# Performance work log

Measured on AMD Instinct MI355X. Metric: run time of the kernel, lower is better.

Reference implementation:

```python
import jax, jax.numpy as jnp
import numpy as np

B, S, D, H = 2, 2048, 1024, 16
Dh = D // H

def setup_inputs() -> dict:
    key = jax.random.key(0)
    ks = jax.random.split(key, 11)
    def lin(k, fan_in):
        bound = 1.0 / np.sqrt(fan_in)
        kw, kb = jax.random.split(k)
        W = jax.random.uniform(kw, (D, D), jnp.float32, -bound, bound)
        b = jax.random.uniform(kb, (D,), jnp.float32, -bound, bound)
        return W, b
    Wq, bq = lin(ks[0], D)
    Wk, bk = lin(ks[1], D)
    Wv, bv = lin(ks[2], D)
    Wo, bo = lin(ks[3], D)
    Q = jax.random.normal(ks[4], (B, S, D), jnp.float32)
    K = jax.random.normal(ks[5], (B, S, D), jnp.float32)
    V = jax.random.normal(ks[6], (B, S, D), jnp.float32)
    return {"Q": Q, "K": K, "V": V, "Wq": Wq, "bq": bq, "Wk": Wk, "bk": bk,
            "Wv": Wv, "bv": bv, "Wo": Wo, "bo": bo}

def _split_heads(x):
    # [B,S,D] -> [B,H,S,Dh]
    b, s, _ = x.shape
    return x.reshape(b, s, H, Dh).transpose(0, 2, 1, 3)

def reference(Q, K, V, Wq, bq, Wk, bk, Wv, bv, Wo, bo):
    q = _split_heads(Q @ Wq.T + bq)
    k = _split_heads(K @ Wk.T + bk)
    v = _split_heads(V @ Wv.T + bv)
    scores = jnp.einsum('bhqd,bhkd->bhqk', q, k) / jnp.sqrt(jnp.float32(Dh))
    attn = jax.nn.softmax(scores, axis=-1)
    out = jnp.einsum('bhqk,bhkd->bhqd', attn, v)  # [B,H,S,Dh]
    out = out.transpose(0, 2, 1, 3).reshape(Q.shape[0], Q.shape[1], D)
    return out @ Wo.T + bo
```

## Files before the change

kernel.cpp:

```cpp
#include <hip/hip_runtime.h>

#define SEQ 2048
#define DMODEL 1024
#define NH 16
#define DH 64

typedef __attribute__((ext_vector_type(8))) short bf16x8;
typedef __attribute__((ext_vector_type(4))) short bf16x4;
typedef __attribute__((ext_vector_type(4))) float floatx4;
typedef __attribute__((ext_vector_type(4))) unsigned short u16x4;
typedef unsigned short u16;
typedef unsigned int u32;

typedef const void __attribute__((address_space(1)))* as1cvp;
typedef void __attribute__((address_space(3)))* as3vp;

__device__ __forceinline__ void glds16(const void* g, void* l) {
    __builtin_amdgcn_global_load_lds((as1cvp)g, (as3vp)l, 16, 0, 0);
}

__device__ __forceinline__ u16 f2bf(float f) {
    union { u32 u; float f; } v; v.f = f;
    return (u16)((v.u + 0x8000u) >> 16);
}

__device__ __forceinline__ u32 pk2(float a, float b) {
    union { u32 u; float f; } x, y; x.f = a; y.f = b;
    u32 xr = x.u + 0x8000u, yr = y.u + 0x8000u;
#if __has_builtin(__builtin_amdgcn_perm)
    return __builtin_amdgcn_perm(yr, xr, 0x07060302u);
#else
    return (xr >> 16) | (yr & 0xffff0000u);
#endif
}

__device__ __forceinline__ float ex2(float x) {
#if __has_builtin(__builtin_amdgcn_exp2f)
    return __builtin_amdgcn_exp2f(x);
#else
    float r; asm("v_exp_f32 %0, %1" : "=v"(r) : "v"(x)); return r;
#endif
}

__device__ __forceinline__ floatx4 mfma16(bf16x4 a, bf16x4 b, floatx4 c) {
#if __has_builtin(__builtin_amdgcn_mfma_f32_16x16x16bf16_1k)
    return __builtin_amdgcn_mfma_f32_16x16x16bf16_1k(a, b, c, 0, 0, 0);
#else
    asm volatile("v_mfma_f32_16x16x16_bf16 %0, %1, %2, %0" : "+v"(c) : "v"(a), "v"(b));
    return c;
#endif
}

__device__ __forceinline__ uint4 cvt8(const float* __restrict__ p) {
    float4 a = *(const float4*)p;
    float4 b = *(const float4*)(p + 4);
    uint4 q;
    q.x = pk2(a.x, a.y); q.y = pk2(a.z, a.w);
    q.z = pk2(b.x, b.y); q.w = pk2(b.z, b.w);
    return q;
}

#define QSCALE 0.18033688011112042f

__global__ __launch_bounds__(256) void cvt_all(
    const float* __restrict__ Q, const float* __restrict__ K, const float* __restrict__ V,
    const float* __restrict__ W0, const float* __restrict__ W1,
    const float* __restrict__ W2, const float* __restrict__ W3,
    u16* __restrict__ Qb, u16* __restrict__ Kb, u16* __restrict__ Vb,
    u16* __restrict__ Wb)
{
    const int y = blockIdx.y;
    const float* src; u16* dst;
    if (y == 0)      { src = Q;  dst = Qb; }
    else if (y == 1) { src = K;  dst = Kb; }
    else if (y == 2) { src = V;  dst = Vb; }
    else {
        if (blockIdx.x >= 512) return;
        src = (y == 3) ? W0 : (y == 4) ? W1 : (y == 5) ? W2 : W3;
        dst = Wb + (size_t)(y - 3) * 1048576;
    }
    size_t i = ((size_t)blockIdx.x * 256 + threadIdx.x) * 8;
    *(uint4*)(dst + i) = cvt8(src + i);
}

__global__ __launch_bounds__(256) void cvt_w(
    const float* __restrict__ W0, const float* __restrict__ W1,
    const float* __restrict__ W2, const float* __restrict__ W3,
    u16* __restrict__ out)
{
    const float* src = (blockIdx.y == 0) ? W0 : (blockIdx.y == 1) ? W1
                     : (blockIdx.y == 2) ? W2 : W3;
    size_t i = ((size_t)blockIdx.x * 256 + threadIdx.x) * 8;
    *(uint4*)(out + (size_t)blockIdx.y * 1048576 + i) = cvt8(src + i);
}

__device__ __forceinline__ void qkv_store(
    int z, u16* __restrict__ outp, int rowg, int col, floatx4 a4, float bv, float sc)
{
    union { u32 w[2]; u16 h[4]; u16x4 v4; } pk;
    pk.w[0] = pk2((a4[0] + bv) * sc, (a4[1] + bv) * sc);
    pk.w[1] = pk2((a4[2] + bv) * sc, (a4[3] + bv) * sc);
    int b = rowg >> 11, s = rowg & 2047, h = col >> 6, d = col & 63;
    if (z < 2) {
#pragma unroll
        for (int r = 0; r < 4; r++)
            outp[((size_t)(b * NH + h) * SEQ + s + r) * DH + d] = pk.h[r];
    } else {
        *(u16x4*)(outp + ((size_t)(b * NH + h) * DH + d) * SEQ + s) = pk.v4;
    }
}

__global__ __launch_bounds__(256) void gemm_qkv_bb(
    const u16* __restrict__ Qb, const u16* __restrict__ Kb, const u16* __restrict__ Vb,
    const u16* __restrict__ Wb,
    const float* __restrict__ b0, const float* __restrict__ b1, const float* __restrict__ b2,
    u16* __restrict__ qo, u16* __restrict__ ko, u16* __restrict__ vto)
{
    __shared__ __align__(16) u16 As[3][4096];
    __shared__ __align__(16) u16 Bs[3][4096];
    const int tid = threadIdx.x, l = tid & 63, w = tid >> 6;
    const int lm = l & 15, quad = l >> 4;
    const int wr = (w >> 1) * 64, wc = (w & 1) * 64;
    const int bm = blockIdx.y * 128, bn = blockIdx.x * 128;
    const int z = blockIdx.z;
    const u16* A      = (z == 0) ? Qb : (z == 1) ? Kb : Vb;
    const u16* W      = Wb + (size_t)z * 1048576;
    const float* bias = (z == 0) ? b0 : (z == 1) ? b1 : b2;

    const int srow = tid >> 2, scol = (tid & 3) * 8;

    floatx4 acc[4][4];
#pragma unroll
    for (int i = 0; i < 4; i++)
#pragma unroll
        for (int j = 0; j < 4; j++) acc[i][j] = (floatx4){0.f, 0.f, 0.f, 0.f};

#define QKV_STAGE(I, NB) do { \
        const int kt_ = (I) * 32; \
        glds16(A + (size_t)(bm + srow) * DMODEL + kt_ + scol, As[NB] + w * 512); \
        glds16(A + (size_t)(bm + 64 + srow) * DMODEL + kt_ + scol, As[NB] + 2048 + w * 512); \
        glds16(W + (size_t)(bn + srow) * DMODEL + kt_ + scol, Bs[NB] + w * 512); \
        glds16(W + (size_t)(bn + 64 + srow) * DMODEL + kt_ + scol, Bs[NB] + 2048 + w * 512); \
    } while (0)

    QKV_STAGE(0, 0);
    QKV_STAGE(1, 1);
    asm volatile("s_waitcnt vmcnt(4)" ::: "memory");
    __builtin_amdgcn_s_barrier();

    int cur = 0, nx = 2;
    for (int i = 0; i < 32; i++) {
        bf16x8 af[4], bfr[4];
#pragma unroll
        for (int mi = 0; mi < 4; mi++)
            af[mi] = *(const bf16x8*)(As[cur] + (wr + mi * 16 + lm) * 32 + quad * 8);
#pragma unroll
        for (int ni = 0; ni < 4; ni++)
            bfr[ni] = *(const bf16x8*)(Bs[cur] + (wc + ni * 16 + lm) * 32 + quad * 8);
#pragma unroll
        for (int mi = 0; mi < 4; mi++)
#pragma unroll
            for (int ni = 0; ni < 4; ni++)
                acc[mi][ni] = __builtin_amdgcn_mfma_f32_16x16x32_bf16(
                    af[mi], bfr[ni], acc[mi][ni], 0, 0, 0);

        if (i + 2 < 32) {
            QKV_STAGE(i + 2, nx);
            asm volatile("s_waitcnt vmcnt(4)" ::: "memory");
            __builtin_amdgcn_s_barrier();
        } else if (i + 1 < 32) {
            asm volatile("s_waitcnt vmcnt(0)" ::: "memory");
            __builtin_amdgcn_s_barrier();
        }
        cur = (cur == 2) ? 0 : cur + 1;
        nx  = (nx == 2) ? 0 : nx + 1;
    }
#undef QKV_STAGE

    const float sc = (z == 0) ? QSCALE : 1.0f;
    u16* outp = (z == 0) ? qo : (z == 1) ? ko : vto;
#pragma unroll
    for (int ni = 0; ni < 4; ni++) {
        int col = bn + wc + ni * 16 + lm;
        float bv = bias[col];
#pragma unroll
        for (int mi = 0; mi < 4; mi++)
            qkv_store(z, outp, bm + wr + mi * 16 + quad * 4, col, acc[mi][ni], bv, sc);
    }
}

template<bool WBF>
__global__ __launch_bounds__(256) void gemm_qkv(
    const float* __restrict__ Qf, const float* __restrict__ Kf, const float* __restrict__ Vf,
    const void* __restrict__ W0, const void* __restrict__ W1, const void* __restrict__ W2,
    const float* __restrict__ b0, const float* __restrict__ b1, const float* __restrict__ b2,
    u16* __restrict__ qo, u16* __restrict__ ko, u16* __restrict__ vto)
{
    __shared__ __align__(16) u16 As[128 * 32];
    __shared__ __align__(16) u16 Bs[128 * 32];
    const int tid = threadIdx.x, l = tid & 63, w = tid >> 6;
    const int lm = l & 15, quad = l >> 4;
    const int wr = (w >> 1) * 64, wc = (w & 1) * 64;
    const int bm = blockIdx.y * 128, bn = blockIdx.x * 128;
    const int z = blockIdx.z;
    const float* A    = (z == 0) ? Qf : (z == 1) ? Kf : Vf;
    const void* Wp    = (z == 0) ? W0 : (z == 1) ? W1 : W2;
    const float* bias = (z == 0) ? b0 : (z == 1) ? b1 : b2;

    floatx4 acc[4][4];
#pragma unroll
    for (int i = 0; i < 4; i++)
#pragma unroll
        for (int j = 0; j < 4; j++) acc[i][j] = (floatx4){0.f, 0.f, 0.f, 0.f};

    for (int kt = 0; kt < DMODEL; kt += 32) {
        __syncthreads();
#pragma unroll
        for (int j = 0; j < 2; j++) {
            int ch = j * 256 + tid, row = ch >> 2, c = ch & 3;
            *(uint4*)(As + ch * 8) = cvt8(A + (size_t)(bm + row) * DMODEL + kt + c * 8);
        }
        if (WBF) {
            const u16* Wb = (const u16*)Wp;
            glds16(Wb + (size_t)(bn + (tid >> 2)) * DMODEL + kt + (tid & 3) * 8, Bs + w * 512);
            glds16(Wb + (size_t)(bn + 64 + (tid >> 2)) * DMODEL + kt + (tid & 3) * 8, Bs + 2048 + w * 512);
        } else {
            const float* Wf = (const float*)Wp;
#pragma unroll
            for (int j = 0; j < 2; j++) {
                int ch = j * 256 + tid, row = ch >> 2, c = ch & 3;
                *(uint4*)(Bs + ch * 8) = cvt8(Wf + (size_t)(bn + row) * DMODEL + kt + c * 8);
            }
        }
        __syncthreads();

        bf16x8 af[4], bfr[4];
#pragma unroll
        for (int mi = 0; mi < 4; mi++)
            af[mi] = *(const bf16x8*)(As + (wr + mi * 16 + lm) * 32 + quad * 8);
#pragma unroll
        for (int ni = 0; ni < 4; ni++)
            bfr[ni] = *(const bf16x8*)(Bs + (wc + ni * 16 + lm) * 32 + quad * 8);
#pragma unroll
        for (int mi = 0; mi < 4; mi++)
#pragma unroll
            for (int ni = 0; ni < 4; ni++)
                acc[mi][ni] = __builtin_amdgcn_mfma_f32_16x16x32_bf16(
                    af[mi], bfr[ni], acc[mi][ni], 0, 0, 0);
    }

    const float sc = (z == 0) ? QSCALE : 1.0f;
    u16* outp = (z == 0) ? qo : (z == 1) ? ko : vto;
#pragma unroll
    for (int ni = 0; ni < 4; ni++) {
        int col = bn + wc + ni * 16 + lm;
        float bv = bias[col];
#pragma unroll
        for (int mi = 0; mi < 4; mi++)
            qkv_store(z, outp, bm + wr + mi * 16 + quad * 4, col, acc[mi][ni], bv, sc);
    }
}

__global__ __launch_bounds__(256) void gemm_o_p(
    const u16* __restrict__ A, const u16* __restrict__ W,
    const float* __restrict__ bias, float* __restrict__ out)
{
    __shared__ __align__(16) u16 As[3][4096];
    __shared__ __align__(16) u16 Bs[3][2048];
    const int tid = threadIdx.x, l = tid & 63, w = tid >> 6;
    const int lm = l & 15, quad = l >> 4;
    const int bm = blockIdx.y * 128, bn = blockIdx.x * 64;

    floatx4 acc[2][4];
#pragma unroll
    for (int i = 0; i < 2; i++)
#pragma unroll
        for (int j = 0; j < 4; j++) acc[i][j] = (floatx4){0.f, 0.f, 0.f, 0.f};

#define O_STAGE(I, NB) do { \
        const int kt_ = (I) * 32; \
        glds16(A + (size_t)(bm + (tid >> 2)) * DMODEL + kt_ + (tid & 3) * 8, As[NB] + w * 512); \
        glds16(A + (size_t)(bm + 64 + (tid >> 2)) * DMODEL + kt_ + (tid & 3) * 8, As[NB] + 2048 + w * 512); \
        glds16(W + (size_t)(bn + (tid >> 2)) * DMODEL + kt_ + (tid & 3) * 8, Bs[NB] + w * 512); \
    } while (0)

    O_STAGE(0, 0);
    O_STAGE(1, 1);
    asm volatile("s_waitcnt vmcnt(3)" ::: "memory");
    __builtin_amdgcn_s_barrier();

    int cur = 0, nx = 2;
    for (int i = 0; i < 32; i++) {
        bf16x8 af[2], bfr[4];
#pragma unroll
        for (int mi = 0; mi < 2; mi++)
            af[mi] = *(const bf16x8*)(As[cur] + (w * 32 + mi * 16 + lm) * 32 + quad * 8);
#pragma unroll
        for (int ni = 0; ni < 4; ni++)
            bfr[ni] = *(const bf16x8*)(Bs[cur] + (ni * 16 + lm) * 32 + quad * 8);
#pragma unroll
        for (int mi = 0; mi < 2; mi++)
#pragma unroll
            for (int ni = 0; ni < 4; ni++)
                acc[mi][ni] = __builtin_amdgcn_mfma_f32_16x16x32_bf16(
                    af[mi], bfr[ni], acc[mi][ni], 0, 0, 0);

        if (i + 2 < 32) {
            O_STAGE(i + 2, nx);
            asm volatile("s_waitcnt vmcnt(3)" ::: "memory");
            __builtin_amdgcn_s_barrier();
        } else if (i + 1 < 32) {
            asm volatile("s_waitcnt vmcnt(0)" ::: "memory");
            __builtin_amdgcn_s_barrier();
        }
        cur = (cur == 2) ? 0 : cur + 1;
        nx  = (nx == 2) ? 0 : nx + 1;
    }
#undef O_STAGE

#pragma unroll
    for (int ni = 0; ni < 4; ni++) {
        int col = bn + ni * 16 + lm;
        float bv = bias[col];
#pragma unroll
        for (int mi = 0; mi < 2; mi++) {
#pragma unroll
            for (int r = 0; r < 4; r++) {
                int rowg = bm + w * 32 + mi * 16 + quad * 4 + r;
                out[(size_t)rowg * DMODEL + col] = acc[mi][ni][r] + bv;
            }
        }
    }
}

template<bool WBF>
__global__ __launch_bounds__(256) void gemm_o(
    const u16* __restrict__ A, const void* __restrict__ Wp,
    const float* __restrict__ bias, float* __restrict__ out)
{
    __shared__ __align__(16) u16 As[128 * 32];
    __shared__ __align__(16) u16 Bs[64 * 32];
    const int tid = threadIdx.x, l = tid & 63, w = tid >> 6;
    const int lm = l & 15, quad = l >> 4;
    const int bm = blockIdx.y * 128, bn = blockIdx.x * 64;

    floatx4 acc[2][4];
#pragma unroll
    for (int i = 0; i < 2; i++)
#pragma unroll
        for (int j = 0; j < 4; j++) acc[i][j] = (floatx4){0.f, 0.f, 0.f, 0.f};

    for (int kt = 0; kt < DMODEL; kt += 32) {
        __syncthreads();
        glds16(A + (size_t)(bm + (tid >> 2)) * DMODEL + kt + (tid & 3) * 8, As + w * 512);
        glds16(A + (size_t)(bm + 64 + (tid >> 2)) * DMODEL + kt + (tid & 3) * 8, As + 2048 + w * 512);
        if (WBF) {
            glds16((const u16*)Wp + (size_t)(bn + (tid >> 2)) * DMODEL + kt + (tid & 3) * 8, Bs + w * 512);
        } else {
            *(uint4*)(Bs + tid * 8) =
                cvt8((const float*)Wp + (size_t)(bn + (tid >> 2)) * DMODEL + kt + (tid & 3) * 8);
        }
        __syncthreads();

        bf16x8 af[2], bfr[4];
#pragma unroll
        for (int mi = 0; mi < 2; mi++)
            af[mi] = *(const bf16x8*)(As + (w * 32 + mi * 16 + lm) * 32 + quad * 8);
#pragma unroll
        for (int ni = 0; ni < 4; ni++)
            bfr[ni] = *(const bf16x8*)(Bs + (ni * 16 + lm) * 32 + quad * 8);
#pragma unroll
        for (int mi = 0; mi < 2; mi++)
#pragma unroll
            for (int ni = 0; ni < 4; ni++)
                acc[mi][ni] = __builtin_amdgcn_mfma_f32_16x16x32_bf16(
                    af[mi], bfr[ni], acc[mi][ni], 0, 0, 0);
    }

#pragma unroll
    for (int ni = 0; ni < 4; ni++) {
        int col = bn + ni * 16 + lm;
        float bv = bias[col];
#pragma unroll
        for (int mi = 0; mi < 2; mi++) {
#pragma unroll
            for (int r = 0; r < 4; r++) {
                int rowg = bm + w * 32 + mi * 16 + quad * 4 + r;
                out[(size_t)rowg * DMODEL + col] = acc[mi][ni][r] + bv;
            }
        }
    }
}

#define SP 72
#define TS (64 * SP)
#define BUFSZ (4 * TS)
__global__ __launch_bounds__(512, 4) void attn_kernel(
    const u16* __restrict__ q, const u16* __restrict__ k,
    const u16* __restrict__ vt, u16* __restrict__ out)
{
    __shared__ __align__(16) u16 smem[2 * BUFSZ];
    const int tid = threadIdx.x, l = tid & 63, w = tid >> 6;
    const int lm = l & 15, quad = l >> 4;
    const int qt = blockIdx.x, bh = blockIdx.y;
    const int b = bh >> 4, h = bh & 15;
    const int rg = w & 3, half = w >> 2;

    bf16x8 qf[2][2];
#pragma unroll
    for (int nt = 0; nt < 2; nt++) {
        int row = qt * 128 + rg * 32 + nt * 16 + lm;
        const u16* qp = q + ((size_t)bh * SEQ + row) * DH;
        qf[nt][0] = *(const bf16x8*)(qp + quad * 8);
        qf[nt][1] = *(const bf16x8*)(qp + 32 + quad * 8);
    }

    floatx4 O[4][2];
#pragma unroll
    for (int dt = 0; dt < 4; dt++)
#pragma unroll
        for (int nt = 0; nt < 2; nt++) O[dt][nt] = (floatx4){0.f, 0.f, 0.f, 0.f};
    floatx4 Ol[2] = {(floatx4){0.f,0.f,0.f,0.f}, (floatx4){0.f,0.f,0.f,0.f}};

    const bf16x4 onesb = {(short)0x3F80, (short)0x3F80, (short)0x3F80, (short)0x3F80};

    const int srow = tid >> 3, scol = (tid & 7) * 8;
    const int pb0 = ((scol >> 2) & 3) * 16 + (scol >> 4) * 4;
    const u16* kbase = k + (size_t)bh * SEQ * DH;
    const u16* vbase = vt + (size_t)bh * DH * SEQ;

    uint4 krA, krB, vrA, vrB;
#define LOADT(T) do { \
        const u16* kg = kbase + (size_t)(T) * 64 * DH; \
        const u16* vg = vbase + (size_t)(T) * 64; \
        krA = *(const uint4*)(kg + (size_t)srow * DH + scol); \
        krB = *(const uint4*)(kg + (size_t)(1024 + srow) * DH + scol); \
        vrA = *(const uint4*)(vg + (size_t)srow * SEQ + scol); \
        vrB = *(const uint4*)(vg + (size_t)srow * SEQ + 1024 + scol); \
    } while (0)
#define WRBUF(BUF) do { \
        u16* K0 = smem + (BUF) * BUFSZ; \
        u16* K1 = K0 + TS; \
        u16* V0 = K0 + 2 * TS; \
        u16* V1 = K0 + 3 * TS; \
        *(uint4*)(K0 + srow * SP + scol) = krA; \
        *(uint4*)(K1 + srow * SP + scol) = krB; \
        *(uint2*)(V0 + srow * SP + pb0)      = make_uint2(vrA.x, vrA.y); \
        *(uint2*)(V0 + srow * SP + pb0 + 16) = make_uint2(vrA.z, vrA.w); \
        *(uint2*)(V1 + srow * SP + pb0)      = make_uint2(vrB.x, vrB.y); \
        *(uint2*)(V1 + srow * SP + pb0 + 16) = make_uint2(vrB.z, vrB.w); \
    } while (0)

    LOADT(0);
    WRBUF(0);
    LOADT(1);
    asm volatile("s_waitcnt lgkmcnt(0)" ::: "memory");
    __builtin_amdgcn_s_barrier();

    for (int t = 0; t < 16; t++) {
        const int cur = t & 1;
        const u16* Kh = smem + cur * BUFSZ + half * TS;
        const u16* Vh = smem + cur * BUFSZ + (2 + half) * TS;

        floatx4 Sc[4][2];
        __builtin_amdgcn_s_setprio(1);
#pragma unroll
        for (int mt = 0; mt < 4; mt++) {
            bf16x8 ka0 = *(const bf16x8*)(Kh + (mt * 16 + lm) * SP + quad * 8);
            bf16x8 ka1 = *(const bf16x8*)(Kh + (mt * 16 + lm) * SP + 32 + quad * 8);
#pragma unroll
            for (int nt = 0; nt < 2; nt++) {
                floatx4 c = (floatx4){0.f, 0.f, 0.f, 0.f};
                c = __builtin_amdgcn_mfma_f32_16x16x32_bf16(ka0, qf[nt][0], c, 0, 0, 0);
                c = __builtin_amdgcn_mfma_f32_16x16x32_bf16(ka1, qf[nt][1], c, 0, 0, 0);
                Sc[mt][nt] = c;
            }
        }
        __builtin_amdgcn_s_setprio(0);

        bf16x4 pb[4][2];
#pragma unroll
        for (int nt = 0; nt < 2; nt++) {
#pragma unroll
            for (int mt = 0; mt < 4; mt++) {
#pragma unroll
                for (int r = 0; r < 4; r++) Sc[mt][nt][r] = ex2(Sc[mt][nt][r]);
                union { u32 w2[2]; bf16x4 v; } pku;
                pku.w2[0] = pk2(Sc[mt][nt][0], Sc[mt][nt][1]);
                pku.w2[1] = pk2(Sc[mt][nt][2], Sc[mt][nt][3]);
                pb[mt][nt] = pku.v;
            }
        }

        __builtin_amdgcn_s_setprio(1);
#pragma unroll
        for (int nt = 0; nt < 2; nt++) {
            Ol[nt] = mfma16(onesb, pb[0][nt], Ol[nt]);
            Ol[nt] = mfma16(onesb, pb[1][nt], Ol[nt]);
            Ol[nt] = mfma16(onesb, pb[2][nt], Ol[nt]);
            Ol[nt] = mfma16(onesb, pb[3][nt], Ol[nt]);
        }

#pragma unroll
        for (int dt = 0; dt < 4; dt++) {
            const u16* vp = Vh + (dt * 16 + lm) * SP + quad * 16;
            bf16x8 v8a = *(const bf16x8*)vp;
            bf16x8 v8b = *(const bf16x8*)(vp + 8);
            bf16x4 va0 = __builtin_shufflevector(v8a, v8a, 0, 1, 2, 3);
            bf16x4 va1 = __builtin_shufflevector(v8a, v8a, 4, 5, 6, 7);
            bf16x4 va2 = __builtin_shufflevector(v8b, v8b, 0, 1, 2, 3);
            bf16x4 va3 = __builtin_shufflevector(v8b, v8b, 4, 5, 6, 7);
            O[dt][0] = mfma16(va0, pb[0][0], O[dt][0]);
            O[dt][1] = mfma16(va0, pb[0][1], O[dt][1]);
            O[dt][0] = mfma16(va1, pb[1][0], O[dt][0]);
            O[dt][1] = mfma16(va1, pb[1][1], O[dt][1]);
            O[dt][0] = mfma16(va2, pb[2][0], O[dt][0]);
            O[dt][1] = mfma16(va2, pb[2][1], O[dt][1]);
            O[dt][0] = mfma16(va3, pb[3][0], O[dt][0]);
            O[dt][1] = mfma16(va3, pb[3][1], O[dt][1]);
        }
        __builtin_amdgcn_s_setprio(0);

        if (t + 1 < 16) {
            asm volatile("s_waitcnt vmcnt(0)" ::: "memory");
            WRBUF(cur ^ 1);
            if (t + 2 < 16) LOADT(t + 2);
        }
        asm volatile("s_waitcnt lgkmcnt(0)" ::: "memory");
        __builtin_amdgcn_s_barrier();
    }
#undef LOADT
#undef WRBUF

    float* obuf  = (float*)smem;
    float* mlbuf = (float*)smem + 8192;
    if (w >= 4) {
#pragma unroll
        for (int nt = 0; nt < 2; nt++) {
            float* ob = obuf + (((rg * 64 + l) * 2 + nt) << 4);
#pragma unroll
            for (int dt = 0; dt < 4; dt++)
                *(floatx4*)(ob + dt * 4) = O[dt][nt];
            mlbuf[(rg * 64 + l) * 2 + nt] = Ol[nt][0];
        }
    }
    __syncthreads();
    if (w < 4) {
#pragma unroll
        for (int nt = 0; nt < 2; nt++) {
            float* ob = obuf + (((rg * 64 + l) * 2 + nt) << 4);
            float lB = mlbuf[(rg * 64 + l) * 2 + nt];
            float inv = 1.0f / (Ol[nt][0] + lB);
            int s = qt * 128 + rg * 32 + nt * 16 + lm;
            u16* op = out + ((size_t)b * SEQ + s) * DMODEL + h * DH;
#pragma unroll
            for (int dt = 0; dt < 4; dt++) {
                floatx4 Ob = *(const floatx4*)(ob + dt * 4);
                union { u32 w2[2]; u16x4 v; } pku;
                pku.w2[0] = pk2((O[dt][nt][0] + Ob[0]) * inv,
                                (O[dt][nt][1] + Ob[1]) * inv);
                pku.w2[1] = pk2((O[dt][nt][2] + Ob[2]) * inv,
                                (O[dt][nt][3] + Ob[3]) * inv);
                *(u16x4*)(op + dt * 16 + quad * 4) = pku.v;
            }
        }
    }
}

extern "C" void kernel_launch(void* const* d_in, const int* in_sizes, int n_in,
                              void* d_out, int out_size, void* d_ws, size_t ws_size,
                              hipStream_t stream) {
    (void)in_sizes; (void)n_in; (void)out_size;
    const float* Q  = (const float*)d_in[0];
    const float* K  = (const float*)d_in[1];
    const float* V  = (const float*)d_in[2];
    const float* Wq = (const float*)d_in[3];
    const float* bq = (const float*)d_in[4];
    const float* Wk = (const float*)d_in[5];
    const float* bk = (const float*)d_in[6];
    const float* Wv = (const float*)d_in[7];
    const float* bv = (const float*)d_in[8];
    const float* Wo = (const float*)d_in[9];
    const float* bo = (const float*)d_in[10];

    const size_t NEL = (size_t)2 * NH * SEQ * DH;
    u16* base = (u16*)d_ws;
    dim3 bb(256);
    dim3 ab(512);

    if (ws_size >= 8 * NEL * 2) {
        u16* Qb   = base;
        u16* Kb   = Qb + NEL;
        u16* Vb   = Kb + NEL;
        u16* Wb   = Vb + NEL;
        u16* qws  = Wb + NEL;
        u16* kws  = qws + NEL;
        u16* vtws = kws + NEL;
        u16* aws  = vtws + NEL;
        cvt_all<<<dim3(2048, 7), bb, 0, stream>>>(Q, K, V, Wq, Wk, Wv, Wo, Qb, Kb, Vb, Wb);
        gemm_qkv_bb<<<dim3(8, 32, 3), bb, 0, stream>>>(
            Qb, Kb, Vb, Wb, bq, bk, bv, qws, kws, vtws);
        attn_kernel<<<dim3(SEQ / 128, 2 * NH), ab, 0, stream>>>(qws, kws, vtws, aws);
        gemm_o_p<<<dim3(16, 32), bb, 0, stream>>>(aws, Wb + 3145728, bo, (float*)d_out);
    } else if (ws_size >= 5 * NEL * 2) {
        u16* Wb = base;
        u16* qws = base + NEL; u16* kws = qws + NEL; u16* vtws = kws + NEL; u16* aws = vtws + NEL;
        cvt_w<<<dim3(512, 4), bb, 0, stream>>>(Wq, Wk, Wv, Wo, Wb);
        gemm_qkv<true><<<dim3(8, 32, 3), bb, 0, stream>>>(
            Q, K, V, Wb, Wb + 1048576, Wb + 2097152, bq, bk, bv, qws, kws, vtws);
        attn_kernel<<<dim3(SEQ / 128, 2 * NH), ab, 0, stream>>>(qws, kws, vtws, aws);
        gemm_o_p<<<dim3(16, 32), bb, 0, stream>>>(aws, Wb + 3145728, bo, (float*)d_out);
    } else {
        u16* qws = base; u16* kws = qws + NEL; u16* vtws = kws + NEL; u16* aws = vtws + NEL;
        gemm_qkv<false><<<dim3(8, 32, 3), bb, 0, stream>>>(
            Q, K, V, Wq, Wk, Wv, bq, bk, bv, qws, kws, vtws);
        attn_kernel<<<dim3(SEQ / 128, 2 * NH), ab, 0, stream>>>(qws, kws, vtws, aws);
        gemm_o<false><<<dim3(16, 32), bb, 0, stream>>>(aws, Wo, bo, (float*)d_out);
    }
}
```

Measured before the change: 227.6 us.

## Fuse fp32-to-bf16 activation conversion into pipelined QKV projection GEMM

Removes the separate pass that converted Q/K/V activations to bf16. The QKV GEMM now reads fp32 activations through registers, packs them to bf16 and writes them to a double-buffered LDS tile, while weight tiles keep using a triple-buffered direct global-to-LDS pipeline. This saves one full write and re-read of the bf16 activations. In exchange the A tiles go through registers, so each K step waits on vmcnt(0), and the kernel asks for two blocks per CU through launch bounds.

After: 249.5 us. +9.6%, slower.

```diff
diff --git a/kernel.cpp b/kernel.cpp
--- a/kernel.cpp
+++ b/kernel.cpp
@@ -61,27 +61,6 @@
 }
 
 #define QSCALE 0.18033688011112042f
-
-__global__ __launch_bounds__(256) void cvt_all(
-    const float* __restrict__ Q, const float* __restrict__ K, const float* __restrict__ V,
-    const float* __restrict__ W0, const float* __restrict__ W1,
-    const float* __restrict__ W2, const float* __restrict__ W3,
-    u16* __restrict__ Qb, u16* __restrict__ Kb, u16* __restrict__ Vb,
-    u16* __restrict__ Wb)
-{
-    const int y = blockIdx.y;
-    const float* src; u16* dst;
-    if (y == 0)      { src = Q;  dst = Qb; }
-    else if (y == 1) { src = K;  dst = Kb; }
-    else if (y == 2) { src = V;  dst = Vb; }
-    else {
-        if (blockIdx.x >= 512) return;
-        src = (y == 3) ? W0 : (y == 4) ? W1 : (y == 5) ? W2 : W3;
-        dst = Wb + (size_t)(y - 3) * 1048576;
-    }
-    size_t i = ((size_t)blockIdx.x * 256 + threadIdx.x) * 8;
-    *(uint4*)(dst + i) = cvt8(src + i);
-}
 
 __global__ __launch_bounds__(256) void cvt_w(
     const float* __restrict__ W0, const float* __restrict__ W1,
@@ -110,24 +89,25 @@
     }
 }
 
-__global__ __launch_bounds__(256) void gemm_qkv_bb(
-    const u16* __restrict__ Qb, const u16* __restrict__ Kb, const u16* __restrict__ Vb,
+__global__ __launch_bounds__(256, 2) void gemm_qkv_f32a(
+    const float* __restrict__ Qf, const float* __restrict__ Kf, const float* __restrict__ Vf,
     const u16* __restrict__ Wb,
     const float* __restrict__ b0, const float* __restrict__ b1, const float* __restrict__ b2,
     u16* __restrict__ qo, u16* __restrict__ ko, u16* __restrict__ vto)
 {
-    __shared__ __align__(16) u16 As[3][4096];
+    __shared__ __align__(16) u16 As[2][4096];
     __shared__ __align__(16) u16 Bs[3][4096];
     const int tid = threadIdx.x, l = tid & 63, w = tid >> 6;
     const int lm = l & 15, quad = l >> 4;
     const int wr = (w >> 1) * 64, wc = (w & 1) * 64;
     const int bm = blockIdx.y * 128, bn = blockIdx.x * 128;
     const int z = blockIdx.z;
-    const u16* A      = (z == 0) ? Qb : (z == 1) ? Kb : Vb;
+    const float* A    = (z == 0) ? Qf : (z == 1) ? Kf : Vf;
     const u16* W      = Wb + (size_t)z * 1048576;
     const float* bias = (z == 0) ? b0 : (z == 1) ? b1 : b2;
 
-    const int srow = tid >> 2, scol = (tid & 3) * 8;
+    const int arow = tid >> 1, acol = (tid & 1) * 16;
+    const int wrow = tid >> 2, wcol = (tid & 3) * 8;
 
     floatx4 acc[4][4];
 #pragma unroll
@@ -135,28 +115,42 @@
 #pragma unroll
         for (int j = 0; j < 4; j++) acc[i][j] = (floatx4){0.f, 0.f, 0.f, 0.f};
 
-#define QKV_STAGE(I, NB) do { \
-        const int kt_ = (I) * 32; \
-        glds16(A + (size_t)(bm + srow) * DMODEL + kt_ + scol, As[NB] + w * 512); \
-        glds16(A + (size_t)(bm + 64 + srow) * DMODEL + kt_ + scol, As[NB] + 2048 + w * 512); \
-        glds16(W + (size_t)(bn + srow) * DMODEL + kt_ + scol, Bs[NB] + w * 512); \
-        glds16(W + (size_t)(bn + 64 + srow) * DMODEL + kt_ + scol, Bs[NB] + 2048 + w * 512); \
+    float4 a0, a1, a2, a3;
+#define LOADA(I) do { \
+        const float* ap = A + (size_t)(bm + arow) * DMODEL + (I) * 32 + acol; \
+        a0 = *(const float4*)ap;       a1 = *(const float4*)(ap + 4); \
+        a2 = *(const float4*)(ap + 8); a3 = *(const float4*)(ap + 12); \
     } while (0)
-
-    QKV_STAGE(0, 0);
-    QKV_STAGE(1, 1);
-    asm volatile("s_waitcnt vmcnt(4)" ::: "memory");
+#define STW(I, NB) do { \
+        glds16(W + (size_t)(bn + wrow) * DMODEL + (I) * 32 + wcol, Bs[NB] + w * 512); \
+        glds16(W + (size_t)(bn + 64 + wrow) * DMODEL + (I) * 32 + wcol, Bs[NB] + 2048 + w * 512); \
+    } while (0)
+#define WRA(NB) do { \
+        uint4 c0, c1; \
+        c0.x = pk2(a0.x, a0.y); c0.y = pk2(a0.z, a0.w); \
+        c0.z = pk2(a1.x, a1.y); c0.w = pk2(a1.z, a1.w); \
+        c1.x = pk2(a2.x, a2.y); c1.y = pk2(a2.z, a2.w); \
+        c1.z = pk2(a3.x, a3.y); c1.w = pk2(a3.z, a3.w); \
+        *(uint4*)(As[NB] + arow * 32 + acol)     = c0; \
+        *(uint4*)(As[NB] + arow * 32 + acol + 8) = c1; \
+    } while (0)
+
+    LOADA(0); STW(0, 0);
+    asm volatile("s_waitcnt vmcnt(0)" ::: "memory");
+    WRA(0);
+    LOADA(1); STW(1, 1);
+    asm volatile("s_waitcnt lgkmcnt(0)" ::: "memory");
     __builtin_amdgcn_s_barrier();
 
-    int cur = 0, nx = 2;
+    int curB = 0;
     for (int i = 0; i < 32; i++) {
         bf16x8 af[4], bfr[4];
 #pragma unroll
         for (int mi = 0; mi < 4; mi++)
-            af[mi] = *(const bf16x8*)(As[cur] + (wr + mi * 16 + lm) * 32 + quad * 8);
+            af[mi] = *(const bf16x8*)(As[i & 1] + (wr + mi * 16 + lm) * 32 + quad * 8);
 #pragma unroll
         for (int ni = 0; ni < 4; ni++)
-            bfr[ni] = *(const bf16x8*)(Bs[cur] + (wc + ni * 16 + lm) * 32 + quad * 8);
+            bfr[ni] = *(const bf16x8*)(Bs[curB] + (wc + ni * 16 + lm) * 32 + quad * 8);
 #pragma unroll
         for (int mi = 0; mi < 4; mi++)
 #pragma unroll
@@ -164,18 +158,22 @@
                 acc[mi][ni] = __builtin_amdgcn_mfma_f32_16x16x32_bf16(
                     af[mi], bfr[ni], acc[mi][ni], 0, 0, 0);
 
-        if (i + 2 < 32) {
-            QKV_STAGE(i + 2, nx);
-            asm volatile("s_waitcnt vmcnt(4)" ::: "memory");
-            __builtin_amdgcn_s_barrier();
-        } else if (i + 1 < 32) {
+        if (i + 1 < 32) {
             asm volatile("s_waitcnt vmcnt(0)" ::: "memory");
-            __builtin_amdgcn_s_barrier();
-        }
-        cur = (cur == 2) ? 0 : cur + 1;
-        nx  = (nx == 2) ? 0 : nx + 1;
-    }
-#undef QKV_STAGE
+            WRA((i + 1) & 1);
+            if (i + 2 < 32) {
+                LOADA(i + 2);
+                int nb = curB + 2; nb = (nb >= 3) ? nb - 3 : nb;
+                STW(i + 2, nb);
+            }
+        }
+        asm volatile("s_waitcnt lgkmcnt(0)" ::: "memory");
+        __builtin_amdgcn_s_barrier();
+        curB = (curB == 2) ? 0 : curB + 1;
+    }
+#undef LOADA
+#undef STW
+#undef WRA
 
     const float sc = (z == 0) ? QSCALE : 1.0f;
     u16* outp = (z == 0) ? qo : (z == 1) ? ko : vto;
@@ -221,9 +219,9 @@
             *(uint4*)(As + ch * 8) = cvt8(A + (size_t)(bm + row) * DMODEL + kt + c * 8);
         }
         if (WBF) {
-            const u16* Wb = (const u16*)Wp;
-            glds16(Wb + (size_t)(bn + (tid >> 2)) * DMODEL + kt + (tid & 3) * 8, Bs + w * 512);
-            glds16(Wb + (size_t)(bn + 64 + (tid >> 2)) * DMODEL + kt + (tid & 3) * 8, Bs + 2048 + w * 512);
+            const u16* Wc = (const u16*)Wp;
+            glds16(Wc + (size_t)(bn + (tid >> 2)) * DMODEL + kt + (tid & 3) * 8, Bs + w * 512);
+            glds16(Wc + (size_t)(bn + 64 + (tid >> 2)) * DMODEL + kt + (tid & 3) * 8, Bs + 2048 + w * 512);
         } else {
             const float* Wf = (const float*)Wp;
 #pragma unroll
@@ -588,26 +586,15 @@
     dim3 bb(256);
     dim3 ab(512);
 
-    if (ws_size >= 8 * NEL * 2) {
-        u16* Qb   = base;
-        u16* Kb   = Qb + NEL;
-        u16* Vb   = Kb + NEL;
-        u16* Wb   = Vb + NEL;
-        u16* qws  = Wb + NEL;
+    if (ws_size >= 5 * NEL * 2) {
+        u16* Wb   = base;
+        u16* qws  = base + NEL;
         u16* kws  = qws + NEL;
         u16* vtws = kws + NEL;
         u16* aws  = vtws + NEL;
-        cvt_all<<<dim3(2048, 7), bb, 0, stream>>>(Q, K, V, Wq, Wk, Wv, Wo, Qb, Kb, Vb, Wb);
-        gemm_qkv_bb<<<dim3(8, 32, 3), bb, 0, stream>>>(
-            Qb, Kb, Vb, Wb, bq, bk, bv, qws, kws, vtws);
-        attn_kernel<<<dim3(SEQ / 128, 2 * NH), ab, 0, stream>>>(qws, kws, vtws, aws);
-        gemm_o_p<<<dim3(16, 32), bb, 0, stream>>>(aws, Wb + 3145728, bo, (float*)d_out);
-    } else if (ws_size >= 5 * NEL * 2) {
-        u16* Wb = base;
-        u16* qws = base + NEL; u16* kws = qws + NEL; u16* vtws = kws + NEL; u16* aws = vtws + NEL;
         cvt_w<<<dim3(512, 4), bb, 0, stream>>>(Wq, Wk, Wv, Wo, Wb);
-        gemm_qkv<true><<<dim3(8, 32, 3), bb, 0, stream>>>(
-            Q, K, V, Wb, Wb + 1048576, Wb + 2097152, bq, bk, bv, qws, kws, vtws);
+        gemm_qkv_f32a<<<dim3(8, 32, 3), bb, 0, stream>>>(
+            Q, K, V, Wb, bq, bk, bv, qws, kws, vtws);
         attn_kernel<<<dim3(SEQ / 128, 2 * NH), ab, 0, stream>>>(qws, kws, vtws, aws);
         gemm_o_p<<<dim3(16, 32), bb, 0, stream>>>(aws, Wb + 3145728, bo, (float*)d_out);
     } else {
```

## Halve attention block to 4 waves, each wave owning 64 query rows

Applied to the files above, without the earlier changes.

The attention kernel drops from 512 to 256 threads per block, and each wave now handles 64 query rows instead of 32. Each K fragment read from shared memory therefore feeds four query tiles instead of two, which halves LDS reads per MFMA and doubles the register-held O and Ol accumulators. Each thread now stages twice as much K/V per tile, and exp/pack work is interleaved per K sub-tile. The cost is higher register pressure and fewer waves per block for hiding latency, with launch bounds lowered to (256,2).

Result: no change. 225.8 us (-0.8%).

```diff
diff --git a/kernel.cpp b/kernel.cpp
--- a/kernel.cpp
+++ b/kernel.cpp
@@ -221,9 +221,9 @@
             *(uint4*)(As + ch * 8) = cvt8(A + (size_t)(bm + row) * DMODEL + kt + c * 8);
         }
         if (WBF) {
-            const u16* Wb = (const u16*)Wp;
-            glds16(Wb + (size_t)(bn + (tid >> 2)) * DMODEL + kt + (tid & 3) * 8, Bs + w * 512);
-            glds16(Wb + (size_t)(bn + 64 + (tid >> 2)) * DMODEL + kt + (tid & 3) * 8, Bs + 2048 + w * 512);
+            const u16* Wc = (const u16*)Wp;
+            glds16(Wc + (size_t)(bn + (tid >> 2)) * DMODEL + kt + (tid & 3) * 8, Bs + w * 512);
+            glds16(Wc + (size_t)(bn + 64 + (tid >> 2)) * DMODEL + kt + (tid & 3) * 8, Bs + 2048 + w * 512);
         } else {
             const float* Wf = (const float*)Wp;
 #pragma unroll
@@ -395,7 +395,7 @@
 #define SP 72
 #define TS (64 * SP)
 #define BUFSZ (4 * TS)
-__global__ __launch_bounds__(512, 4) void attn_kernel(
+__global__ __launch_bounds__(256, 2) void attn_kernel(
     const u16* __restrict__ q, const u16* __restrict__ k,
     const u16* __restrict__ vt, u16* __restrict__ out)
 {
@@ -404,51 +404,60 @@
     const int lm = l & 15, quad = l >> 4;
     const int qt = blockIdx.x, bh = blockIdx.y;
     const int b = bh >> 4, h = bh & 15;
-    const int rg = w & 3, half = w >> 2;
-
-    bf16x8 qf[2][2];
-#pragma unroll
-    for (int nt = 0; nt < 2; nt++) {
-        int row = qt * 128 + rg * 32 + nt * 16 + lm;
+    const int rg = w & 1, half = w >> 1;
+
+    bf16x8 qf[4][2];
+#pragma unroll
+    for (int nt = 0; nt < 4; nt++) {
+        int row = qt * 128 + rg * 64 + nt * 16 + lm;
         const u16* qp = q + ((size_t)bh * SEQ + row) * DH;
         qf[nt][0] = *(const bf16x8*)(qp + quad * 8);
         qf[nt][1] = *(const bf16x8*)(qp + 32 + quad * 8);
     }
 
-    floatx4 O[4][2];
+    floatx4 O[4][4];
 #pragma unroll
     for (int dt = 0; dt < 4; dt++)
 #pragma unroll
-        for (int nt = 0; nt < 2; nt++) O[dt][nt] = (floatx4){0.f, 0.f, 0.f, 0.f};
-    floatx4 Ol[2] = {(floatx4){0.f,0.f,0.f,0.f}, (floatx4){0.f,0.f,0.f,0.f}};
+        for (int nt = 0; nt < 4; nt++) O[dt][nt] = (floatx4){0.f, 0.f, 0.f, 0.f};
+    floatx4 Ol[4];
+#pragma unroll
+    for (int nt = 0; nt < 4; nt++) Ol[nt] = (floatx4){0.f, 0.f, 0.f, 0.f};
 
     const bf16x4 onesb = {(short)0x3F80, (short)0x3F80, (short)0x3F80, (short)0x3F80};
 
-    const int srow = tid >> 3, scol = (tid & 7) * 8;
-    const int pb0 = ((scol >> 2) & 3) * 16 + (scol >> 4) * 4;
+    const int srow = tid >> 2, sc4 = tid & 3;
     const u16* kbase = k + (size_t)bh * SEQ * DH;
     const u16* vbase = vt + (size_t)bh * DH * SEQ;
 
-    uint4 krA, krB, vrA, vrB;
+    uint4 kA0, kA1, kB0, kB1, vA0, vA1, vB0, vB1;
 #define LOADT(T) do { \
-        const u16* kg = kbase + (size_t)(T) * 64 * DH; \
-        const u16* vg = vbase + (size_t)(T) * 64; \
-        krA = *(const uint4*)(kg + (size_t)srow * DH + scol); \
-        krB = *(const uint4*)(kg + (size_t)(1024 + srow) * DH + scol); \
-        vrA = *(const uint4*)(vg + (size_t)srow * SEQ + scol); \
-        vrB = *(const uint4*)(vg + (size_t)srow * SEQ + 1024 + scol); \
+        const u16* kgA = kbase + (size_t)((T) * 64 + srow) * DH + sc4 * 16; \
+        const u16* kgB = kbase + (size_t)(1024 + (T) * 64 + srow) * DH + sc4 * 16; \
+        kA0 = *(const uint4*)kgA;       kA1 = *(const uint4*)(kgA + 8); \
+        kB0 = *(const uint4*)kgB;       kB1 = *(const uint4*)(kgB + 8); \
+        const u16* vgA = vbase + (size_t)srow * SEQ + (T) * 64 + sc4 * 16; \
+        const u16* vgB = vgA + 1024; \
+        vA0 = *(const uint4*)vgA;       vA1 = *(const uint4*)(vgA + 8); \
+        vB0 = *(const uint4*)vgB;       vB1 = *(const uint4*)(vgB + 8); \
     } while (0)
 #define WRBUF(BUF) do { \
         u16* K0 = smem + (BUF) * BUFSZ; \
         u16* K1 = K0 + TS; \
         u16* V0 = K0 + 2 * TS; \
         u16* V1 = K0 + 3 * TS; \
-        *(uint4*)(K0 + srow * SP + scol) = krA; \
-        *(uint4*)(K1 + srow * SP + scol) = krB; \
-        *(uint2*)(V0 + srow * SP + pb0)      = make_uint2(vrA.x, vrA.y); \
-        *(uint2*)(V0 + srow * SP + pb0 + 16) = make_uint2(vrA.z, vrA.w); \
-        *(uint2*)(V1 + srow * SP + pb0)      = make_uint2(vrB.x, vrB.y); \
-        *(uint2*)(V1 + srow * SP + pb0 + 16) = make_uint2(vrB.z, vrB.w); \
+        *(uint4*)(K0 + srow * SP + sc4 * 16)     = kA0; \
+        *(uint4*)(K0 + srow * SP + sc4 * 16 + 8) = kA1; \
+        *(uint4*)(K1 + srow * SP + sc4 * 16)     = kB0; \
+        *(uint4*)(K1 + srow * SP + sc4 * 16 + 8) = kB1; \
+        *(uint2*)(V0 + srow * SP + 0 * 16 + sc4 * 4) = make_uint2(vA0.x, vA0.y); \
+        *(uint2*)(V0 + srow * SP + 1 * 16 + sc4 * 4) = make_uint2(vA0.z, vA0.w); \
+        *(uint2*)(V0 + srow * SP + 2 * 16 + sc4 * 4) = make_uint2(vA1.x, vA1.y); \
+        *(uint2*)(V0 + srow * SP + 3 * 16 + sc4 * 4) = make_uint2(vA1.z, vA1.w); \
+        *(uint2*)(V1 + srow * SP + 0 * 16 + sc4 * 4) = make_uint2(vB0.x, vB0.y); \
+        *(uint2*)(V1 + srow * SP + 1 * 16 + sc4 * 4) = make_uint2(vB0.z, vB0.w); \
+        *(uint2*)(V1 + srow * SP + 2 * 16 + sc4 * 4) = make_uint2(vB1.x, vB1.y); \
+        *(uint2*)(V1 + srow * SP + 3 * 16 + sc4 * 4) = make_uint2(vB1.z, vB1.w); \
     } while (0)
 
     LOADT(0);
@@ -462,39 +471,35 @@
         const u16* Kh = smem + cur * BUFSZ + half * TS;
         const u16* Vh = smem + cur * BUFSZ + (2 + half) * TS;
 
-        floatx4 Sc[4][2];
-        __builtin_amdgcn_s_setprio(1);
+        bf16x4 pb[4][4];
 #pragma unroll
         for (int mt = 0; mt < 4; mt++) {
             bf16x8 ka0 = *(const bf16x8*)(Kh + (mt * 16 + lm) * SP + quad * 8);
             bf16x8 ka1 = *(const bf16x8*)(Kh + (mt * 16 + lm) * SP + 32 + quad * 8);
-#pragma unroll
-            for (int nt = 0; nt < 2; nt++) {
+            floatx4 Sc[4];
+            __builtin_amdgcn_s_setprio(1);
+#pragma unroll
+            for (int nt = 0; nt < 4; nt++) {
                 floatx4 c = (floatx4){0.f, 0.f, 0.f, 0.f};
                 c = __builtin_amdgcn_mfma_f32_16x16x32_bf16(ka0, qf[nt][0], c, 0, 0, 0);
                 c = __builtin_amdgcn_mfma_f32_16x16x32_bf16(ka1, qf[nt][1], c, 0, 0, 0);
-                Sc[mt][nt] = c;
+                Sc[nt] = c;
             }
-        }
-        __builtin_amdgcn_s_setprio(0);
-
-        bf16x4 pb[4][2];
-#pragma unroll
-        for (int nt = 0; nt < 2; nt++) {
-#pragma unroll
-            for (int mt = 0; mt < 4; mt++) {
-#pragma unroll
-                for (int r = 0; r < 4; r++) Sc[mt][nt][r] = ex2(Sc[mt][nt][r]);
+            __builtin_amdgcn_s_setprio(0);
+#pragma unroll
+            for (int nt = 0; nt < 4; nt++) {
+#pragma unroll
+                for (int r = 0; r < 4; r++) Sc[nt][r] = ex2(Sc[nt][r]);
                 union { u32 w2[2]; bf16x4 v; } pku;
-                pku.w2[0] = pk2(Sc[mt][nt][0], Sc[mt][nt][1]);
-                pku.w2[1] = pk2(Sc[mt][nt][2], Sc[mt][nt][3]);
+                pku.w2[0] = pk2(Sc[nt][0], Sc[nt][1]);
+                pku.w2[1] = pk2(Sc[nt][2], Sc[nt][3]);
                 pb[mt][nt] = pku.v;
             }
         }
 
         __builtin_amdgcn_s_setprio(1);
 #pragma unroll
-        for (int nt = 0; nt < 2; nt++) {
+        for (int nt = 0; nt < 4; nt++) {
             Ol[nt] = mfma16(onesb, pb[0][nt], Ol[nt]);
             Ol[nt] = mfma16(onesb, pb[1][nt], Ol[nt]);
             Ol[nt] = mfma16(onesb, pb[2][nt], Ol[nt]);
@@ -510,14 +515,13 @@
             bf16x4 va1 = __builtin_shufflevector(v8a, v8a, 4, 5, 6, 7);
             bf16x4 va2 = __builtin_shufflevector(v8b, v8b, 0, 1, 2, 3);
             bf16x4 va3 = __builtin_shufflevector(v8b, v8b, 4, 5, 6, 7);
-            O[dt][0] = mfma16(va0, pb[0][0], O[dt][0]);
-            O[dt][1] = mfma16(va0, pb[0][1], O[dt][1]);
-            O[dt][0] = mfma16(va1, pb[1][0], O[dt][0]);
-            O[dt][1] = mfma16(va1, pb[1][1], O[dt][1]);
-            O[dt][0] = mfma16(va2, pb[2][0], O[dt][0]);
-            O[dt][1] = mfma16(va2, pb[2][1], O[dt][1]);
-            O[dt][0] = mfma16(va3, pb[3][0], O[dt][0]);
-            O[dt][1] = mfma16(va3, pb[3][1], O[dt][1]);
+#pragma unroll
+            for (int nt = 0; nt < 4; nt++) {
+                O[dt][nt] = mfma16(va0, pb[0][nt], O[dt][nt]);
+                O[dt][nt] = mfma16(va1, pb[1][nt], O[dt][nt]);
+                O[dt][nt] = mfma16(va2, pb[2][nt], O[dt][nt]);
+                O[dt][nt] = mfma16(va3, pb[3][nt], O[dt][nt]);
+            }
         }
         __builtin_amdgcn_s_setprio(0);
 
@@ -534,24 +538,24 @@
 
     float* obuf  = (float*)smem;
     float* mlbuf = (float*)smem + 8192;
-    if (w >= 4) {
-#pragma unroll
-        for (int nt = 0; nt < 2; nt++) {
-            float* ob = obuf + (((rg * 64 + l) * 2 + nt) << 4);
+    if (w >= 2) {
+#pragma unroll
+        for (int nt = 0; nt < 4; nt++) {
+            float* ob = obuf + (((rg * 64 + l) * 4 + nt) << 4);
 #pragma unroll
             for (int dt = 0; dt < 4; dt++)
                 *(floatx4*)(ob + dt * 4) = O[dt][nt];
-            mlbuf[(rg * 64 + l) * 2 + nt] = Ol[nt][0];
+            mlbuf[(rg * 64 + l) * 4 + nt] = Ol[nt][0];
         }
     }
     __syncthreads();
-    if (w < 4) {
-#pragma unroll
-        for (int nt = 0; nt < 2; nt++) {
-            float* ob = obuf + (((rg * 64 + l) * 2 + nt) << 4);
-            float lB = mlbuf[(rg * 64 + l) * 2 + nt];
+    if (w < 2) {
+#pragma unroll
+        for (int nt = 0; nt < 4; nt++) {
+            float* ob = obuf + (((rg * 64 + l) * 4 + nt) << 4);
+            float lB = mlbuf[(rg * 64 + l) * 4 + nt];
             float inv = 1.0f / (Ol[nt][0] + lB);
-            int s = qt * 128 + rg * 32 + nt * 16 + lm;
+            int s = qt * 128 + rg * 64 + nt * 16 + lm;
             u16* op = out + ((size_t)b * SEQ + s) * DMODEL + h * DH;
 #pragma unroll
             for (int dt = 0; dt < 4; dt++) {
@@ -586,7 +590,7 @@
     const size_t NEL = (size_t)2 * NH * SEQ * DH;
     u16* base = (u16*)d_ws;
     dim3 bb(256);
-    dim3 ab(512);
+    dim3 ab(256);
 
     if (ws_size >= 8 * NEL * 2) {
         u16* Qb   = base;
```
